# Kernel tuning notes

Measured on AMD Instinct MI355X. Metric: run time of the kernel, lower is better.

## Reference

```python
import jax, jax.numpy as jnp
import numpy as np

B, N, L, C, H = 4, 4096, 1024, 1024, 16
D = C // H  # head_dim = 64
SCALE = 1.0 / np.sqrt(D)


def setup_inputs() -> dict:
    key = jax.random.key(0)
    ks = jax.random.split(key, 5)
    return {
        "x": jax.random.normal(ks[0], (B, N, C), dtype=jnp.float32),
        "query": jax.random.normal(ks[1], (B, L, C), dtype=jnp.float32),
        "Wq": jax.random.normal(ks[2], (C, C), dtype=jnp.float32) * 0.02,
        "Wkv": jax.random.normal(ks[3], (2 * C, C), dtype=jnp.float32) * 0.02,
        "Wproj": jax.random.normal(ks[4], (C, C), dtype=jnp.float32) * 0.02,
        "bproj": jnp.zeros((C,), dtype=jnp.float32),
    }


def reference(x, query, Wq, Wkv, Wproj, bproj):
    # q projection: [B,L,C] -> [B,H,L,D]
    q = (query @ Wq.T).reshape(B, L, H, D).transpose(0, 2, 1, 3)
    # kv projection: [B,N,2C] -> k,v each [B,H,N,D]
    kv = (x @ Wkv.T).reshape(B, N, 2, H, D).transpose(2, 0, 3, 1, 4)
    k, v = kv[0], kv[1]
    # unfused SDPA: explicit [B,H,L,N] score matrix (faithful to source)
    attn = jnp.einsum('bhld,bhnd->bhln', q, k) * SCALE
    attn = jax.nn.softmax(attn, axis=-1)
    out = jnp.einsum('bhln,bhnd->bhld', attn, v)  # [B,H,L,D]
    out = out.transpose(0, 2, 1, 3).reshape(B, L, C)
    return out @ Wproj.T + bproj
```

## Files before the change

### kernel.cpp

```cpp
#include <hip/hip_runtime.h>
#include <hip/hip_bf16.h>

typedef __attribute__((ext_vector_type(8))) short short8;
typedef __attribute__((ext_vector_type(4))) float floatx4;

#if __has_builtin(__builtin_amdgcn_exp2f)
#define EXP2(x) __builtin_amdgcn_exp2f(x)
#else
#define EXP2(x) exp2f(x)
#endif

#define BAR() __builtin_amdgcn_s_barrier()
#define FENCE() asm volatile("" ::: "memory")
#define WAIT_LGKM0() asm volatile("s_waitcnt lgkmcnt(0)" ::: "memory")
#define WAIT_VM(n) asm volatile("s_waitcnt vmcnt(" #n ")" ::: "memory")

__device__ __forceinline__ short f2bf(float f) {
  __hip_bfloat16 h = __float2bfloat16(f);
  return *reinterpret_cast<const short*>(&h);
}

__device__ __forceinline__ short8 cvt_f32x8_bf16(const float* __restrict__ p) {
  float4 a = *reinterpret_cast<const float4*>(p);
  float4 b = *reinterpret_cast<const float4*>(p + 4);
  short8 r;
  r[0] = f2bf(a.x); r[1] = f2bf(a.y); r[2] = f2bf(a.z); r[3] = f2bf(a.w);
  r[4] = f2bf(b.x); r[5] = f2bf(b.y); r[6] = f2bf(b.z); r[7] = f2bf(b.w);
  return r;
}

typedef const __attribute__((address_space(1))) void* gptr1;
typedef __attribute__((address_space(3))) void* lptr3;
__device__ __forceinline__ void gl_lds16(const void* g, void* l) {
  __builtin_amdgcn_global_load_lds((gptr1)g, (lptr3)l, 16, 0, 0);
}

__global__ __launch_bounds__(256)
void f32_to_bf16(const float* __restrict__ in, short* __restrict__ out, int n8) {
  int i = blockIdx.x * blockDim.x + threadIdx.x;
  if (i < n8) {
    short8 v = cvt_f32x8_bf16(in + (size_t)i * 8);
    *reinterpret_cast<short8*>(out + (size_t)i * 8) = v;
  }
}

__global__ __launch_bounds__(512, 2)
void gemm256_kv(const short* __restrict__ A, const short* __restrict__ B,
                short* __restrict__ k_out, short* __restrict__ vt,
                int M, int N, int K)
{
  __shared__ __align__(16) short lds[2][2][2][128 * 64];

  const int tid  = threadIdx.x;
  const int lane = tid & 63;
  const int w    = tid >> 6;
  const int wm   = w >> 2;
  const int wn   = w & 3;
  const int cl   = lane & 15;
  const int hi   = lane >> 4;
  const int srl  = lane >> 3;
  const int gch8 = (((lane & 7) ^ srl) << 3);

  const int ntile = N >> 8;
  int bid = blockIdx.x;
  { int cpx = gridDim.x >> 3; bid = (bid & 7) * cpx + (bid >> 3); }
  const int tm = bid / ntile, tn = bid % ntile;
  const int m0 = tm << 8, n0 = tn << 8;
  const int NT = K >> 6;

  auto stageA = [&](int par, int slot, int ktX) {
    #pragma unroll
    for (int j = 0; j < 2; ++j) {
      const int sr = (w << 4) + (j << 3) + srl;
      const int tr = ((sr >> 6) << 7) + (slot << 6) + (sr & 63);
      gl_lds16(A + (size_t)(m0 + tr) * K + ktX + gch8,
               (void*)&lds[par][0][slot][((w << 4) + (j << 3)) * 64]);
    }
  };
  auto stageB = [&](int par, int slot, int ktX) {
    #pragma unroll
    for (int j = 0; j < 2; ++j) {
      const int sr = (w << 4) + (j << 3) + srl;
      const int tr = ((sr >> 5) << 6) + (slot << 5) + (sr & 31);
      gl_lds16(B + (size_t)(n0 + tr) * K + ktX + gch8,
               (void*)&lds[par][1][slot][((w << 4) + (j << 3)) * 64]);
    }
  };

  const floatx4 fzero = {0.f, 0.f, 0.f, 0.f};
  floatx4 acc[8][4];
  #pragma unroll
  for (int m = 0; m < 8; ++m)
    #pragma unroll
    for (int n = 0; n < 4; ++n)
      acc[m][n] = fzero;

  short8 af[4][2], b0[2][2], b1[2][2];

  auto readA = [&](int par, int slot) {
    #pragma unroll
    for (int m = 0; m < 4; ++m)
      #pragma unroll
      for (int ks = 0; ks < 2; ++ks) {
        const int sr = (wm << 6) + (m << 4) + cl;
        const int cpos = ((((ks << 2) + hi) ^ (sr & 7)) << 3);
        af[m][ks] = *reinterpret_cast<const short8*>(&lds[par][0][slot][sr * 64 + cpos]);
      }
  };
  auto readB = [&](int par, int slot, short8 (&bf)[2][2]) {
    #pragma unroll
    for (int n = 0; n < 2; ++n)
      #pragma unroll
      for (int ks = 0; ks < 2; ++ks) {
        const int sr = (wn << 5) + (n << 4) + cl;
        const int cpos = ((((ks << 2) + hi) ^ (sr & 7)) << 3);
        bf[n][ks] = *reinterpret_cast<const short8*>(&lds[par][1][slot][sr * 64 + cpos]);
      }
  };

  #define QUAD(BF, MH, NH)                                                     \
    __builtin_amdgcn_s_setprio(1);                                             \
    _Pragma("unroll")                                                          \
    for (int ks = 0; ks < 2; ++ks)                                             \
      _Pragma("unroll")                                                        \
      for (int m = 0; m < 4; ++m)                                              \
        _Pragma("unroll")                                                      \
        for (int n = 0; n < 2; ++n)                                            \
          acc[(MH)*4 + m][(NH)*2 + n] = __builtin_amdgcn_mfma_f32_16x16x32_bf16( \
              af[m][ks], BF[n][ks], acc[(MH)*4 + m][(NH)*2 + n], 0, 0, 0);     \
    __builtin_amdgcn_s_setprio(0);

  stageA(0, 0, 0); stageB(0, 0, 0); stageB(0, 1, 0); stageA(0, 1, 0);
  stageA(1, 0, 64); stageB(1, 0, 64); stageB(1, 1, 64);
  WAIT_VM(6); BAR(); FENCE();

  for (int t = 0; t < NT; ++t) {
    const int p  = t & 1;
    const int pn = p ^ 1;
    int t1 = t + 1; if (t1 >= NT) t1 -= NT;
    int t2 = t + 2; if (t2 >= NT) t2 -= NT;
    const int kt1 = t1 << 6;
    const int kt2 = t2 << 6;

    readA(p, 0); readB(p, 0, b0);
    stageA(pn, 1, kt1);
    BAR(); WAIT_LGKM0();
    QUAD(b0, 0, 0);
    BAR(); FENCE();

    readB(p, 1, b1);
    stageA(p, 0, kt2);
    BAR(); WAIT_LGKM0();
    QUAD(b1, 0, 1);
    BAR(); FENCE();

    readA(p, 1);
    stageB(p, 0, kt2);
    BAR(); WAIT_LGKM0();
    QUAD(b0, 1, 0);
    BAR(); FENCE();

    stageB(p, 1, kt2);
    WAIT_VM(6);
    BAR(); WAIT_LGKM0();
    QUAD(b1, 1, 1);
    BAR(); FENCE();
  }
  WAIT_VM(0);

  const int rq = hi << 2;
  #pragma unroll
  for (int Mi = 0; Mi < 8; ++Mi) {
    #pragma unroll
    for (int Nn = 0; Nn < 4; ++Nn) {
      const int grow = m0 + wm * 128 + Mi * 16 + rq;
      const int gcol = n0 + wn * 64 + Nn * 16 + cl;
      if (gcol < 1024) {
        #pragma unroll
        for (int i = 0; i < 4; ++i)
          k_out[(size_t)(grow + i) * 1024 + gcol] = f2bf(acc[Mi][Nn][i]);
      } else {
        const int d  = gcol - 1024;
        const int bb = grow >> 12;
        const int nn = grow & 4095;
        size_t base = ((size_t)(bb * 16 + (d >> 6)) * 64 + (d & 63)) * 4096 + nn;
        short4 pk;
        pk.x = f2bf(acc[Mi][Nn][0]); pk.y = f2bf(acc[Mi][Nn][1]);
        pk.z = f2bf(acc[Mi][Nn][2]); pk.w = f2bf(acc[Mi][Nn][3]);
        *reinterpret_cast<short4*>(&vt[base]) = pk;
      }
    }
  }
}

template<int MODE>
__global__ __launch_bounds__(256, 2)
void gemm_bt(const short* __restrict__ A, const short* __restrict__ B,
             void* __restrict__ O0, const float* __restrict__ bias,
             int M, int N, int K, float oscale)
{
  __shared__ short As[128 * 64];
  __shared__ short Bs[128 * 64];

  const int tid  = threadIdx.x;
  const int lane = tid & 63;
  const int w    = tid >> 6;
  const int ntile = N >> 7;
  int bid = blockIdx.x;
  { int cpx = gridDim.x >> 3; bid = (bid & 7) * cpx + (bid >> 3); }
  const int tm = bid / ntile;
  const int tn = bid % ntile;
  const int m0 = tm << 7, n0 = tn << 7;
  const int wr = (w >> 1) << 6;
  const int wc = (w & 1) << 6;

  const int srow = lane >> 3;
  const int scol = (lane & 7) << 3;

  const floatx4 fzero = {0.f, 0.f, 0.f, 0.f};
  floatx4 acc[4][4];
  #pragma unroll
  for (int m = 0; m < 4; ++m)
    #pragma unroll
    for (int n = 0; n < 4; ++n)
      acc[m][n] = fzero;

  for (int kt = 0; kt < K; kt += 64) {
    #pragma unroll
    for (int i = 0; i < 4; ++i) {
      const int chunk = (w << 2) + i;
      const int row   = (chunk << 3) + srow;
      gl_lds16(A + (size_t)(m0 + row) * K + kt + scol, &As[chunk * 512]);
      gl_lds16(B + (size_t)(n0 + row) * K + kt + scol, &Bs[chunk * 512]);
    }
    __syncthreads();

    #pragma unroll
    for (int ks = 0; ks < 2; ++ks) {
      short8 af[4], bfr[4];
      #pragma unroll
      for (int m = 0; m < 4; ++m)
        af[m] = *reinterpret_cast<const short8*>(
            &As[(wr + m * 16 + (lane & 15)) * 64 + ks * 32 + ((lane >> 4) << 3)]);
      #pragma unroll
      for (int n = 0; n < 4; ++n)
        bfr[n] = *reinterpret_cast<const short8*>(
            &Bs[(wc + n * 16 + (lane & 15)) * 64 + ks * 32 + ((lane >> 4) << 3)]);
      #pragma unroll
      for (int m = 0; m < 4; ++m)
        #pragma unroll
        for (int n = 0; n < 4; ++n)
          acc[m][n] = __builtin_amdgcn_mfma_f32_16x16x32_bf16(af[m], bfr[n], acc[m][n], 0, 0, 0);
    }
    __syncthreads();
  }

  const int rq = (lane >> 4) << 2;
  const int cl = lane & 15;
  #pragma unroll
  for (int m = 0; m < 4; ++m) {
    #pragma unroll
    for (int n = 0; n < 4; ++n) {
      const int grow = m0 + wr + m * 16 + rq;
      const int gcol = n0 + wc + n * 16 + cl;
      if (MODE == 0) {
        short* o = (short*)O0;
        #pragma unroll
        for (int i = 0; i < 4; ++i)
          o[(size_t)(grow + i) * N + gcol] = f2bf(acc[m][n][i] * oscale);
      } else {
        float* o = (float*)O0;
        const float bv = bias[gcol];
        #pragma unroll
        for (int i = 0; i < 4; ++i)
          o[(size_t)(grow + i) * N + gcol] = acc[m][n][i] + bv;
      }
    }
  }
}

__global__ __launch_bounds__(256, 2)
void attn_fwd(const short* __restrict__ q_ws, const short* __restrict__ k_ws,
              const short* __restrict__ vt_ws, short* __restrict__ ao_ws)
{
  __shared__ short Ks[64 * 64];
  __shared__ short Vts[64 * 64];
  __shared__ short Pl[4][32 * 64];

  const int tid  = threadIdx.x;
  const int lane = tid & 63;
  const int w    = tid >> 6;
  const int bh = blockIdx.x >> 3;
  const int qt = blockIdx.x & 7;
  const int b  = bh >> 4;
  const int h  = bh & 15;
  const int q0 = qt * 128 + w * 32;
  const int cl = lane & 15;
  const int rq = (lane >> 4) << 2;

  short8 qf[2][2];
  #pragma unroll
  for (int t = 0; t < 2; ++t)
    #pragma unroll
    for (int ks = 0; ks < 2; ++ks) {
      size_t idx = (size_t)(b * 1024 + q0 + t * 16 + cl) * 1024
                 + h * 64 + ks * 32 + ((lane >> 4) << 3);
      qf[t][ks] = *reinterpret_cast<const short8*>(&q_ws[idx]);
    }

  const floatx4 fzero = {0.f, 0.f, 0.f, 0.f};
  floatx4 o[2][4];
  float lr[2] = {0.f, 0.f};
  #pragma unroll
  for (int m = 0; m < 2; ++m)
    #pragma unroll
    for (int nd = 0; nd < 4; ++nd) o[m][nd] = fzero;

  const int sr  = tid >> 2;
  const int sc  = (tid & 3) << 4;
  const int sch = sc >> 3;
  const int ssw = sr & 7;

  const int hi4   = (lane >> 4) << 2;
  const int pwoff = hi4 & 4;
  const int pwc   = hi4 >> 3;

  for (int kv0 = 0; kv0 < 4096; kv0 += 64) {
    {
      const short* ksrc = k_ws + (size_t)(b * 4096 + kv0 + sr) * 1024 + h * 64 + sc;
      short8 v0 = *reinterpret_cast<const short8*>(ksrc);
      short8 v1 = *reinterpret_cast<const short8*>(ksrc + 8);
      *reinterpret_cast<short8*>(&Ks[sr * 64 + ((sch ^ ssw) << 3)]) = v0;
      *reinterpret_cast<short8*>(&Ks[sr * 64 + (((sch + 1) ^ ssw) << 3)]) = v1;
      const short* vsrc = vt_ws + ((size_t)bh * 64 + sr) * 4096 + kv0 + sc;
      short8 u0 = *reinterpret_cast<const short8*>(vsrc);
      short8 u1 = *reinterpret_cast<const short8*>(vsrc + 8);
      *reinterpret_cast<short8*>(&Vts[sr * 64 + ((sch ^ ssw) << 3)]) = u0;
      *reinterpret_cast<short8*>(&Vts[sr * 64 + (((sch + 1) ^ ssw) << 3)]) = u1;
    }
    __syncthreads();

    floatx4 s[4][2];
    #pragma unroll
    for (int n = 0; n < 4; ++n)
      #pragma unroll
      for (int t = 0; t < 2; ++t) s[n][t] = fzero;
    __builtin_amdgcn_s_setprio(1);
    #pragma unroll
    for (int ks = 0; ks < 2; ++ks) {
      short8 kf[4];
      #pragma unroll
      for (int n = 0; n < 4; ++n) {
        int row = n * 16 + cl;
        int ch  = ((ks << 2) + (lane >> 4)) ^ (row & 7);
        kf[n] = *reinterpret_cast<const short8*>(&Ks[row * 64 + (ch << 3)]);
      }
      #pragma unroll
      for (int n = 0; n < 4; ++n)
        #pragma unroll
        for (int t = 0; t < 2; ++t)
          s[n][t] = __builtin_amdgcn_mfma_f32_16x16x32_bf16(kf[n], qf[t][ks], s[n][t], 0, 0, 0);
    }
    __builtin_amdgcn_s_setprio(0);

    #pragma unroll
    for (int t = 0; t < 2; ++t) {
      const int qrow = t * 16 + cl;
      const int base = qrow * 64;
      const int key  = qrow & 7;
      #pragma unroll
      for (int n = 0; n < 4; ++n) {
        short4 pk;
        #pragma unroll
        for (int i = 0; i < 4; ++i) {
          float p = EXP2(s[n][t][i]);
          lr[t] += p;
          pk[i] = f2bf(p);
        }
        const int ch = ((n << 1) + pwc) ^ key;
        *reinterpret_cast<short4*>(&Pl[w][base + (ch << 3) + pwoff]) = pk;
      }
    }

    __builtin_amdgcn_s_setprio(1);
    #pragma unroll
    for (int ks = 0; ks < 2; ++ks) {
      short8 pa[2], vf[4];
      #pragma unroll
      for (int m = 0; m < 2; ++m) {
        int row = m * 16 + cl;
        int ch  = ((ks << 2) + (lane >> 4)) ^ (row & 7);
        pa[m] = *reinterpret_cast<const short8*>(&Pl[w][row * 64 + (ch << 3)]);
      }
      #pragma unroll
      for (int nd = 0; nd < 4; ++nd) {
        int row = nd * 16 + cl;
        int ch  = ((ks << 2) + (lane >> 4)) ^ (row & 7);
        vf[nd] = *reinterpret_cast<const short8*>(&Vts[row * 64 + (ch << 3)]);
      }
      #pragma unroll
      for (int m = 0; m < 2; ++m)
        #pragma unroll
        for (int nd = 0; nd < 4; ++nd)
          o[m][nd] = __builtin_amdgcn_mfma_f32_16x16x32_bf16(pa[m], vf[nd], o[m][nd], 0, 0, 0);
    }
    __builtin_amdgcn_s_setprio(0);
    __syncthreads();
  }

  float lf[2];
  #pragma unroll
  for (int t = 0; t < 2; ++t) {
    float l = lr[t];
    l += __shfl_xor(l, 16);
    l += __shfl_xor(l, 32);
    lf[t] = l;
  }
  #pragma unroll
  for (int m = 0; m < 2; ++m) {
    float inv[4];
    #pragma unroll
    for (int i = 0; i < 4; ++i)
      inv[i] = 1.f / __shfl(lf[m], rq + i);
    #pragma unroll
    for (int nd = 0; nd < 4; ++nd)
      #pragma unroll
      for (int i = 0; i < 4; ++i) {
        size_t idx = (size_t)(b * 1024 + q0 + m * 16 + rq + i) * 1024
                   + h * 64 + nd * 16 + cl;
        ao_ws[idx] = f2bf(o[m][nd][i] * inv[i]);
      }
  }
}

extern "C" void kernel_launch(void* const* d_in, const int* in_sizes, int n_in,
                              void* d_out, int out_size, void* d_ws, size_t ws_size,
                              hipStream_t stream)
{
  const float* x     = (const float*)d_in[0];
  const float* query = (const float*)d_in[1];
  const float* Wq    = (const float*)d_in[2];
  const float* Wkv   = (const float*)d_in[3];
  const float* Wproj = (const float*)d_in[4];
  const float* bproj = (const float*)d_in[5];
  float* out = (float*)d_out;

  const float QSCALE = 0.18033688011112042f;

  char* ws = (char*)d_ws;
  short* k_ws   = (short*)(ws);
  short* vt_ws  = (short*)(ws + (32ull << 20));
  short* xb     = (short*)(ws + (64ull << 20));
  short* qb     = (short*)(ws + (64ull << 20));
  short* q_ws   = (short*)(ws + (72ull << 20));
  short* ao_ws  = (short*)(ws + (80ull << 20));
  short* wkvb   = (short*)(ws + (96ull << 20));
  short* wqb    = (short*)(ws + (100ull << 20));
  short* wprojb = (short*)(ws + (102ull << 20));

  f32_to_bf16<<<dim3(1024), 256, 0, stream>>>(Wkv,   wkvb,   (2048 * 1024) / 8);
  f32_to_bf16<<<dim3(512),  256, 0, stream>>>(Wq,    wqb,    (1024 * 1024) / 8);
  f32_to_bf16<<<dim3(512),  256, 0, stream>>>(Wproj, wprojb, (1024 * 1024) / 8);
  f32_to_bf16<<<dim3(8192), 256, 0, stream>>>(x,     xb,     (16384 * 1024) / 8);

  gemm256_kv<<<dim3(512), 512, 0, stream>>>(xb, wkvb, k_ws, vt_ws,
                                            16384, 2048, 1024);
  f32_to_bf16<<<dim3(2048), 256, 0, stream>>>(query, qb, (4096 * 1024) / 8);
  gemm_bt<0><<<dim3(256), 256, 0, stream>>>(qb, wqb, q_ws, nullptr,
                                            4096, 1024, 1024, QSCALE);
  attn_fwd<<<dim3(512), 256, 0, stream>>>(q_ws, k_ws, vt_ws, ao_ws);
  gemm_bt<2><<<dim3(256), 256, 0, stream>>>(ao_ws, wprojb, out, bproj,
                                            4096, 1024, 1024, 1.0f);
}
```

Before: 240.6 us.

## Double-buffer K/V tiles with direct global-to-LDS loads and remap block order

The attention kernel now stages K and V^T tiles straight into two LDS buffers through a gl_lds16 helper, prefetching the next tile while the current one is computed. Raw vmcnt waits and barriers replace __syncthreads, which removes the register round-trip and the load stall at the top of each iteration. Blocks are also remapped so that consecutive block IDs cover different batch-heads, which spreads K/V reuse differently across L2 and XCDs. The cost is twice the K/V LDS footprint, which may affect occupancy at two blocks per CU, and one redundant prefetch on the final iteration.

```diff
diff --git a/kernel.cpp b/kernel.cpp
--- a/kernel.cpp
+++ b/kernel.cpp
@@ -283,15 +283,16 @@
 void attn_fwd(const short* __restrict__ q_ws, const short* __restrict__ k_ws,
               const short* __restrict__ vt_ws, short* __restrict__ ao_ws)
 {
-  __shared__ short Ks[64 * 64];
-  __shared__ short Vts[64 * 64];
+  __shared__ __align__(16) short Ks[2][64 * 64];
+  __shared__ __align__(16) short Vts[2][64 * 64];
   __shared__ short Pl[4][32 * 64];
 
   const int tid  = threadIdx.x;
   const int lane = tid & 63;
   const int w    = tid >> 6;
-  const int bh = blockIdx.x >> 3;
-  const int qt = blockIdx.x & 7;
+  const int i    = blockIdx.x;
+  const int bh   = (i & 7) * 8 + (i >> 6);
+  const int qt   = (i >> 3) & 7;
   const int b  = bh >> 4;
   const int h  = bh & 15;
   const int q0 = qt * 128 + w * 32;
@@ -316,35 +317,36 @@
     #pragma unroll
     for (int nd = 0; nd < 4; ++nd) o[m][nd] = fzero;
 
-  const int sr  = tid >> 2;
-  const int sc  = (tid & 3) << 4;
-  const int sch = sc >> 3;
-  const int ssw = sr & 7;
+  const int c0    = w << 1;
+  const int srow8 = lane >> 3;
+  const int gch8  = (((lane & 7) ^ srow8) << 3);
+  const short* kbase = k_ws + (size_t)(b * 4096 + (c0 << 3) + srow8) * 1024 + h * 64 + gch8;
+  const short* vbase = vt_ws + ((size_t)bh * 64 + (c0 << 3) + srow8) * 4096 + gch8;
+
+  auto stage = [&](int buf, int kv0) {
+    gl_lds16(kbase + (size_t)kv0 * 1024,          (void*)&Ks[buf][c0 * 512]);
+    gl_lds16(kbase + (size_t)kv0 * 1024 + 8192,   (void*)&Ks[buf][(c0 + 1) * 512]);
+    gl_lds16(vbase + kv0,                          (void*)&Vts[buf][c0 * 512]);
+    gl_lds16(vbase + kv0 + 8 * 4096,               (void*)&Vts[buf][(c0 + 1) * 512]);
+  };
 
   const int hi4   = (lane >> 4) << 2;
   const int pwoff = hi4 & 4;
   const int pwc   = hi4 >> 3;
 
-  for (int kv0 = 0; kv0 < 4096; kv0 += 64) {
-    {
-      const short* ksrc = k_ws + (size_t)(b * 4096 + kv0 + sr) * 1024 + h * 64 + sc;
-      short8 v0 = *reinterpret_cast<const short8*>(ksrc);
-      short8 v1 = *reinterpret_cast<const short8*>(ksrc + 8);
-      *reinterpret_cast<short8*>(&Ks[sr * 64 + ((sch ^ ssw) << 3)]) = v0;
-      *reinterpret_cast<short8*>(&Ks[sr * 64 + (((sch + 1) ^ ssw) << 3)]) = v1;
-      const short* vsrc = vt_ws + ((size_t)bh * 64 + sr) * 4096 + kv0 + sc;
-      short8 u0 = *reinterpret_cast<const short8*>(vsrc);
-      short8 u1 = *reinterpret_cast<const short8*>(vsrc + 8);
-      *reinterpret_cast<short8*>(&Vts[sr * 64 + ((sch ^ ssw) << 3)]) = u0;
-      *reinterpret_cast<short8*>(&Vts[sr * 64 + (((sch + 1) ^ ssw) << 3)]) = u1;
-    }
-    __syncthreads();
+  stage(0, 0);
+  for (int t = 0; t < 64; ++t) {
+    const int cur = t & 1;
+    const int nt  = (t + 1) & 63;
+    stage(cur ^ 1, nt << 6);
+    WAIT_VM(4);
+    BAR(); FENCE();
 
     floatx4 s[4][2];
     #pragma unroll
     for (int n = 0; n < 4; ++n)
       #pragma unroll
-      for (int t = 0; t < 2; ++t) s[n][t] = fzero;
+      for (int tt = 0; tt < 2; ++tt) s[n][tt] = fzero;
     __builtin_amdgcn_s_setprio(1);
     #pragma unroll
     for (int ks = 0; ks < 2; ++ks) {
@@ -353,29 +355,29 @@
       for (int n = 0; n < 4; ++n) {
         int row = n * 16 + cl;
         int ch  = ((ks << 2) + (lane >> 4)) ^ (row & 7);
-        kf[n] = *reinterpret_cast<const short8*>(&Ks[row * 64 + (ch << 3)]);
+        kf[n] = *reinterpret_cast<const short8*>(&Ks[cur][row * 64 + (ch << 3)]);
       }
       #pragma unroll
       for (int n = 0; n < 4; ++n)
         #pragma unroll
-        for (int t = 0; t < 2; ++t)
-          s[n][t] = __builtin_amdgcn_mfma_f32_16x16x32_bf16(kf[n], qf[t][ks], s[n][t], 0, 0, 0);
+        for (int tt = 0; tt < 2; ++tt)
+          s[n][tt] = __builtin_amdgcn_mfma_f32_16x16x32_bf16(kf[n], qf[tt][ks], s[n][tt], 0, 0, 0);
     }
     __builtin_amdgcn_s_setprio(0);
 
     #pragma unroll
-    for (int t = 0; t < 2; ++t) {
-      const int qrow = t * 16 + cl;
+    for (int tt = 0; tt < 2; ++tt) {
+      const int qrow = tt * 16 + cl;
       const int base = qrow * 64;
       const int key  = qrow & 7;
       #pragma unroll
       for (int n = 0; n < 4; ++n) {
         short4 pk;
         #pragma unroll
-        for (int i = 0; i < 4; ++i) {
-          float p = EXP2(s[n][t][i]);
-          lr[t] += p;
-          pk[i] = f2bf(p);
+        for (int ii = 0; ii < 4; ++ii) {
+          float p = EXP2(s[n][tt][ii]);
+          lr[tt] += p;
+          pk[ii] = f2bf(p);
         }
         const int ch = ((n << 1) + pwc) ^ key;
         *reinterpret_cast<short4*>(&Pl[w][base + (ch << 3) + pwoff]) = pk;
@@ -396,7 +398,7 @@
       for (int nd = 0; nd < 4; ++nd) {
         int row = nd * 16 + cl;
         int ch  = ((ks << 2) + (lane >> 4)) ^ (row & 7);
-        vf[nd] = *reinterpret_cast<const short8*>(&Vts[row * 64 + (ch << 3)]);
+        vf[nd] = *reinterpret_cast<const short8*>(&Vts[cur][row * 64 + (ch << 3)]);
       }
       #pragma unroll
       for (int m = 0; m < 2; ++m)
@@ -405,8 +407,9 @@
           o[m][nd] = __builtin_amdgcn_mfma_f32_16x16x32_bf16(pa[m], vf[nd], o[m][nd], 0, 0, 0);
     }
     __builtin_amdgcn_s_setprio(0);
-    __syncthreads();
-  }
+    BAR(); FENCE();
+  }
+  WAIT_VM(0);
 
   float lf[2];
   #pragma unroll
@@ -420,15 +423,15 @@
   for (int m = 0; m < 2; ++m) {
     float inv[4];
     #pragma unroll
-    for (int i = 0; i < 4; ++i)
-      inv[i] = 1.f / __shfl(lf[m], rq + i);
+    for (int ii = 0; ii < 4; ++ii)
+      inv[ii] = 1.f / __shfl(lf[m], rq + ii);
     #pragma unroll
     for (int nd = 0; nd < 4; ++nd)
       #pragma unroll
-      for (int i = 0; i < 4; ++i) {
-        size_t idx = (size_t)(b * 1024 + q0 + m * 16 + rq + i) * 1024
+      for (int ii = 0; ii < 4; ++ii) {
+        size_t idx = (size_t)(b * 1024 + q0 + m * 16 + rq + ii) * 1024
                    + h * 64 + nd * 16 + cl;
-        ao_ws[idx] = f2bf(o[m][nd][i] * inv[i]);
+        ao_ws[idx] = f2bf(o[m][nd][ii] * inv[ii]);
       }
   }
 }
```

After: 234.0 us. 2.8% less time.
